# Optimization experiments

Hardware: AMD Instinct MI355X
Metric: run time of the kernel (lower is better)

The kernel has to match this reference:

```python
import jax, jax.numpy as jnp
import numpy as np

NEG = -9e15  # matches -9000000000000000.0 in the torch source


def setup_inputs() -> dict:
    key = jax.random.key(0)
    k1, k2, k3, k4 = jax.random.split(key, 4)
    N, F_in, F_out = 8192, 512, 64
    h = jax.random.normal(k1, (N, F_in), dtype=jnp.float32)
    adj = jax.random.randint(k2, (N, N), 0, 2, dtype=jnp.int32)
    # xavier_uniform with gain=1.414
    def xavier(k, shape, gain=1.414):
        fan_in, fan_out = shape[0], shape[1]
        bound = gain * np.sqrt(6.0 / (fan_in + fan_out))
        return jax.random.uniform(k, shape, dtype=jnp.float32, minval=-bound, maxval=bound)
    W = xavier(k3, (F_in, F_out))
    a = xavier(k4, (2 * F_out, 1))
    return {"h": h, "adj": adj, "W": W, "a": a}


def reference(h, adj, W, a):
    alpha = 0.2
    F_out = W.shape[1]
    Wh = h.astype(jnp.float32) @ W                      # [N, F_out]
    # e[i,j] = leakyrelu( Wh[i] . a[:F_out] + Wh[j] . a[F_out:] )
    Wh1 = Wh @ a[:F_out, :]                             # [N, 1]
    Wh2 = Wh @ a[F_out:, :]                             # [N, 1]
    e = jax.nn.leaky_relu(Wh1 + Wh2.T, negative_slope=alpha)  # [N, N]
    scores = jnp.where(adj > 0, e, NEG)                 # mask non-edges
    attention = jax.nn.softmax(scores, axis=1)          # row softmax
    h_prime = attention @ Wh                            # [N, F_out]
    return h_prime
```

## Files before the change

### kernel.cpp

```cpp
#include <hip/hip_runtime.h>
#include <cstdint>
#include <cstddef>


#define GAT_N    8192
#define GAT_FIN  512
#define GAT_F    64
#define TJ       64
#define JSPLIT   16
#define JCHUNK   (GAT_N / JSPLIT)
#define NTILES   (JCHUNK / TJ)
#define NWORDS   (GAT_N / 64)

typedef __attribute__((ext_vector_type(8))) short short8;
typedef __attribute__((ext_vector_type(4))) float f32x4;

__device__ __forceinline__ float lrelu(float x) { return fmaxf(x, 0.2f * x); }

__device__ __forceinline__ unsigned enc_f32(float f) {
    unsigned b = __float_as_uint(f);
    return b ^ ((b & 0x80000000u) ? 0xFFFFFFFFu : 0x80000000u);
}
__device__ __forceinline__ float dec_f32(unsigned u) {
    return __uint_as_float(u ^ ((u & 0x80000000u) ? 0x80000000u : 0xFFFFFFFFu));
}
__device__ __forceinline__ short f2bf_trunc(float f) {
    return (short)(__float_as_uint(f) >> 16);
}
__device__ __forceinline__ float bfhi(float f) {
    return __uint_as_float(__float_as_uint(f) & 0xFFFF0000u);
}

__device__ __forceinline__ void gload_lds16(const void* g, void* l) {
    __builtin_amdgcn_global_load_lds(
        (const __attribute__((address_space(1))) void*)g,
        (__attribute__((address_space(3))) void*)l, 16, 0, 0);
}

__global__ __launch_bounds__(256) void k_pack(
    const int* __restrict__ adj, unsigned long long* __restrict__ packed)
{
    const int lane = threadIdx.x & 63;
    const int wv   = blockIdx.x * 4 + (threadIdx.x >> 6);
    const size_t wbase = (size_t)wv * 256;
    for (int it = 0; it < 32; ++it) {
        const size_t w0 = wbase + (size_t)it * 8;
        const int* src = adj + w0 * 64 + lane;
        unsigned long long b0, b1, b2, b3, b4, b5, b6, b7;
        b0 = __ballot(src[0 * 64] > 0);
        b1 = __ballot(src[1 * 64] > 0);
        b2 = __ballot(src[2 * 64] > 0);
        b3 = __ballot(src[3 * 64] > 0);
        b4 = __ballot(src[4 * 64] > 0);
        b5 = __ballot(src[5 * 64] > 0);
        b6 = __ballot(src[6 * 64] > 0);
        b7 = __ballot(src[7 * 64] > 0);
        if (lane == 0) {
            ulonglong2* dst = (ulonglong2*)&packed[w0];
            dst[0] = {b0, b1};
            dst[1] = {b2, b3};
            dst[2] = {b4, b5};
            dst[3] = {b6, b7};
        }
    }
}

__global__ __launch_bounds__(256) void k_wh(
    const float* __restrict__ h, const float* __restrict__ W,
    const float* __restrict__ a,
    float* __restrict__ wh1, float* __restrict__ wh2,
    unsigned int* __restrict__ mw2,
    unsigned short* __restrict__ whtHi, unsigned short* __restrict__ whtLo)
{
    __shared__ float sW[2][64 * GAT_F];
    __shared__ unsigned short sTh[GAT_F][16];
    __shared__ unsigned short sTl[GAT_F][16];
    __shared__ unsigned int smax[16];
    const int tid  = threadIdx.x;
    const int lane = tid & 63;
    const int wq   = __builtin_amdgcn_readfirstlane(tid >> 6);
    const size_t r0 = (size_t)blockIdx.x * 16;
    const int rp = tid >> 4;
    const int f4 = (tid & 15) * 4;

    int Bg[4];
#pragma unroll
    for (int c = 0; c < 4; ++c) Bg[c] = wq * 64 + c * 256;

    const char* wsrc = (const char*)W;
    {
        char* dst = (char*)sW[0];
#pragma unroll
        for (int c = 0; c < 4; ++c)
            gload_lds16(wsrc + (size_t)(Bg[c] + lane) * 16, dst + Bg[c] * 16);
    }

    const float* ha = h + (r0 + rp) * GAT_FIN;
    float4 acc = {0.f, 0.f, 0.f, 0.f};

    for (int ck = 0; ck < 8; ++ck) {
        __syncthreads();
        if (ck + 1 < 8) {
            const char* src = wsrc + (size_t)(ck + 1) * 16384;
            char* dst = (char*)sW[(ck + 1) & 1];
#pragma unroll
            for (int c = 0; c < 4; ++c)
                gload_lds16(src + (size_t)(Bg[c] + lane) * 16, dst + Bg[c] * 16);
        }
        const float* wcp = sW[ck & 1];
#pragma unroll 4
        for (int k4 = 0; k4 < 16; ++k4) {
            float4 hv = *(const float4*)&ha[ck * 64 + k4 * 4];
            const float* hvf = (const float*)&hv;
#pragma unroll
            for (int kk = 0; kk < 4; ++kk) {
                float4 wv = *(const float4*)&wcp[(k4 * 4 + kk) * GAT_F + f4];
                acc.x = fmaf(hvf[kk], wv.x, acc.x);
                acc.y = fmaf(hvf[kk], wv.y, acc.y);
                acc.z = fmaf(hvf[kk], wv.z, acc.z);
                acc.w = fmaf(hvf[kk], wv.w, acc.w);
            }
        }
    }

    float4 a1 = *(const float4*)&a[f4];
    float4 a2 = *(const float4*)&a[GAT_F + f4];
    float pa = acc.x*a1.x + acc.y*a1.y + acc.z*a1.z + acc.w*a1.w;
    float pb = acc.x*a2.x + acc.y*a2.y + acc.z*a2.z + acc.w*a2.w;
#pragma unroll
    for (int m = 1; m < 16; m <<= 1) {
        pa += __shfl_xor(pa, m);
        pb += __shfl_xor(pb, m);
    }
    if ((tid & 15) == 0) {
        wh1[r0 + rp] = pa;
        wh2[r0 + rp] = pb;
        smax[rp] = enc_f32(pb);
    }

    const float* af = (const float*)&acc;
#pragma unroll
    for (int e = 0; e < 4; ++e) {
        float v = af[e];
        sTh[f4 + e][rp] = (unsigned short)f2bf_trunc(v);
        sTl[f4 + e][rp] = (unsigned short)f2bf_trunc(v - bfhi(v));
    }
    __syncthreads();

    {
        const int f = tid >> 2, rq = tid & 3;
        uint2 vh = *(const uint2*)&sTh[f][rq * 4];
        uint2 vl = *(const uint2*)&sTl[f][rq * 4];
        *(uint2*)&whtHi[(size_t)f * GAT_N + r0 + rq * 4] = vh;
        *(uint2*)&whtLo[(size_t)f * GAT_N + r0 + rq * 4] = vl;
    }
    if (tid == 0) {
        unsigned m = smax[0];
#pragma unroll
        for (int r = 1; r < 16; ++r) m = max(m, smax[r]);
        atomicMax(mw2, m);
    }
}

__global__ __launch_bounds__(256, 4) void k_attend(
    const unsigned long long* __restrict__ packed,
    const unsigned short* __restrict__ whtHi,
    const unsigned short* __restrict__ whtLo,
    const float* __restrict__ wh1, const float* __restrict__ wh2,
    const unsigned int* __restrict__ mw2,
    float* __restrict__ po, float* __restrict__ pl)
{
    __shared__ char sB[2][16384];

    const int tid  = threadIdx.x;
    const int w    = tid >> 6;
    const int lane = tid & 63;
    const int wq   = __builtin_amdgcn_readfirstlane(w);
    const int fl   = lane & 15;
    const int jg   = lane >> 4;
    const int rw   = blockIdx.x * 64 + w * 16;
    const int j0   = blockIdx.y * JCHUNK;

    const float Mw2 = dec_f32(*mw2);
    const float ai  = wh1[rw + fl];
    const float Mi  = lrelu(ai + Mw2);

    const char* ssrc[4]; int sdstu[4];
#pragma unroll
    for (int c = 0; c < 4; ++c) {
        const int Bgc = wq * 64 + (c & 1) * 256;
        const int G   = Bgc + lane;
        const int f = G >> 3, g = G & 7;
        const unsigned short* base = (c < 2) ? whtHi : whtLo;
        ssrc[c]  = (const char*)(base + (size_t)f * GAT_N + j0 + ((g ^ (f & 7)) * 8));
        sdstu[c] = ((c < 2) ? 0 : 8192) + Bgc * 16;
    }

    const int off0 = fl * 128 + (((0 * 4 + jg) ^ (fl & 7)) * 16);
    const int off1 = fl * 128 + (((1 * 4 + jg) ^ (fl & 7)) * 16);

    const unsigned long long* mp = packed + (size_t)(rw + fl) * NWORDS + (j0 >> 6);
    const float* wp = wh2 + j0 + jg * 8;

    {
#pragma unroll
        for (int c = 0; c < 4; ++c)
            gload_lds16(ssrc[c], (char*)sB[0] + sdstu[c]);
    }
    unsigned long long amc = mp[0];
    float4 wc[4];
#pragma unroll
    for (int q = 0; q < 4; ++q)
        wc[q] = *(const float4*)(wp + (q >> 1) * 32 + (q & 1) * 4);

    f32x4 acc[4] = {};
    float psum = 0.f;

    for (int t = 0; t < NTILES; ++t) {
        const int cur = t & 1;
        __syncthreads();

        if (t + 1 < NTILES) {
#pragma unroll
            for (int c = 0; c < 4; ++c)
                gload_lds16(ssrc[c] + (size_t)(t + 1) * 128,
                            (char*)sB[cur ^ 1] + sdstu[c]);
        }
        const int tn = (t + 1 < NTILES) ? t + 1 : t;
        unsigned long long amn = mp[tn];
        float4 wn[4];
#pragma unroll
        for (int q = 0; q < 4; ++q)
            wn[q] = *(const float4*)(wp + tn * TJ + (q >> 1) * 32 + (q & 1) * 4);

        const char* sbc = sB[cur];
#pragma unroll
        for (int s = 0; s < 2; ++s) {
            const unsigned m8 = (unsigned)(amc >> (s * 32 + jg * 8)) & 0xFFu;
            float pv[8];
#pragma unroll
            for (int hh = 0; hh < 2; ++hh) {
                const float* bvf = (const float*)&wc[s * 2 + hh];
#pragma unroll
                for (int e = 0; e < 4; ++e) {
                    float sc = lrelu(ai + bvf[e]);
                    float pe = __expf(sc - Mi);
                    pv[hh * 4 + e] = ((m8 >> (hh * 4 + e)) & 1u) ? pe : 0.f;
                }
            }
            short8 ph, plo;
#pragma unroll
            for (int e = 0; e < 8; ++e) {
                psum  += pv[e];
                ph[e]  = f2bf_trunc(pv[e]);
                plo[e] = f2bf_trunc(pv[e] - bfhi(pv[e]));
            }
            const int offs = s ? off1 : off0;
#pragma unroll
            for (int nb = 0; nb < 4; ++nb) {
                short8 bh = *(const short8*)(sbc + offs + nb * 2048);
                short8 bl = *(const short8*)(sbc + 8192 + offs + nb * 2048);
                acc[nb] = __builtin_amdgcn_mfma_f32_16x16x32_bf16(ph,  bh, acc[nb], 0, 0, 0);
                acc[nb] = __builtin_amdgcn_mfma_f32_16x16x32_bf16(plo, bh, acc[nb], 0, 0, 0);
                acc[nb] = __builtin_amdgcn_mfma_f32_16x16x32_bf16(ph,  bl, acc[nb], 0, 0, 0);
            }
        }
        amc = amn;
#pragma unroll
        for (int q = 0; q < 4; ++q) wc[q] = wn[q];
    }

    psum += __shfl_xor(psum, 16);
    psum += __shfl_xor(psum, 32);
    if (lane < 16)
        pl[(size_t)blockIdx.y * GAT_N + rw + lane] = psum;

    const size_t ob = ((size_t)blockIdx.y * GAT_N + rw + jg * 4) * GAT_F + fl;
#pragma unroll
    for (int nb = 0; nb < 4; ++nb) {
#pragma unroll
        for (int r = 0; r < 4; ++r)
            po[ob + (size_t)r * GAT_F + nb * 16] = acc[nb][r];
    }
}

__global__ __launch_bounds__(256) void k_merge(
    const float* __restrict__ po, const float* __restrict__ pl,
    float* __restrict__ out)
{
    const int idx = blockIdx.x * 256 + threadIdx.x;
    const int i = idx >> 6;
    float s = 0.f, ls = 0.f;
#pragma unroll
    for (int y = 0; y < JSPLIT; ++y) {
        s  += po[(size_t)y * GAT_N * GAT_F + idx];
        ls += pl[(size_t)y * GAT_N + i];
    }
    out[idx] = s / ls;
}

extern "C" void kernel_launch(void* const* d_in, const int* in_sizes, int n_in,
                              void* d_out, int out_size, void* d_ws, size_t ws_size,
                              hipStream_t stream) {
    (void)in_sizes; (void)n_in; (void)out_size; (void)ws_size;
    const float* h   = (const float*)d_in[0];
    const int*   adj = (const int*)d_in[1];
    const float* W   = (const float*)d_in[2];
    const float* a   = (const float*)d_in[3];
    float* out = (float*)d_out;

    char* wsb = (char*)d_ws;
    float*              wh1    = (float*)(wsb);
    float*              wh2    = (float*)(wsb + 32768);
    unsigned int*       mw2    = (unsigned int*)(wsb + 65536);
    unsigned long long* packed = (unsigned long long*)(wsb + 131072);
    unsigned short*     whtHi  = (unsigned short*)(wsb + 8519680);
    unsigned short*     whtLo  = (unsigned short*)(wsb + 9568256);
    float*              po     = (float*)(wsb + 10616832);
    float*              pl     = (float*)(wsb + 44171264);

    hipMemsetAsync(mw2, 0, 4, stream);
    k_pack  <<<1024, 256, 0, stream>>>(adj, packed);
    k_wh    <<<GAT_N / 16, 256, 0, stream>>>(h, W, a, wh1, wh2, mw2, whtHi, whtLo);
    k_attend<<<dim3(GAT_N / 64, JSPLIT), 256, 0, stream>>>(packed, whtHi, whtLo,
                                                           wh1, wh2, mw2, po, pl);
    k_merge <<<GAT_N * GAT_F / 256, 256, 0, stream>>>(po, pl, out);
}
```

Before: 451.6 us.

## Pre-pack Wh into MFMA fragment layout and load B operands directly from global

```diff
diff --git a/kernel.cpp b/kernel.cpp
--- a/kernel.cpp
+++ b/kernel.cpp
@@ -35,6 +35,10 @@
     __builtin_amdgcn_global_load_lds(
         (const __attribute__((address_space(1))) void*)g,
         (__attribute__((address_space(3))) void*)l, 16, 0, 0);
+}
+
+__device__ __forceinline__ short8 as_short8(const int4& v) {
+    union { int4 i; short8 s; } u; u.i = v; return u.s;
 }
 
 __global__ __launch_bounds__(256) void k_pack(
@@ -70,7 +74,7 @@
     const float* __restrict__ a,
     float* __restrict__ wh1, float* __restrict__ wh2,
     unsigned int* __restrict__ mw2,
-    unsigned short* __restrict__ whtHi, unsigned short* __restrict__ whtLo)
+    char* __restrict__ pbHi, char* __restrict__ pbLo)
 {
     __shared__ float sW[2][64 * GAT_F];
     __shared__ unsigned short sTh[GAT_F][16];
@@ -148,11 +152,21 @@
     __syncthreads();
 
     {
-        const int f = tid >> 2, rq = tid & 3;
-        uint2 vh = *(const uint2*)&sTh[f][rq * 4];
-        uint2 vl = *(const uint2*)&sTl[f][rq * 4];
-        *(uint2*)&whtHi[(size_t)f * GAT_N + r0 + rq * 4] = vh;
-        *(uint2*)&whtLo[(size_t)f * GAT_N + r0 + rq * 4] = vl;
+        const int tt  = blockIdx.x >> 2;
+        const int q   = blockIdx.x & 3;
+        const int s   = q >> 1;
+        const int hf  = tid >> 7;
+        const int rem = tid & 127;
+        const int nb  = rem >> 5;
+        const int jgo = (rem >> 4) & 1;
+        const int fl  = rem & 15;
+        const int jga = (q & 1) * 2 + jgo;
+        const unsigned short* st = hf ? &sTl[nb * 16 + fl][jgo * 8]
+                                      : &sTh[nb * 16 + fl][jgo * 8];
+        uint4 v = *(const uint4*)st;
+        char* base = hf ? pbLo : pbHi;
+        *(uint4*)(base + (size_t)tt * 8192 + s * 4096 + nb * 1024
+                       + (jga * 16 + fl) * 16) = v;
     }
     if (tid == 0) {
         unsigned m = smax[0];
@@ -162,20 +176,16 @@
     }
 }
 
-__global__ __launch_bounds__(256, 4) void k_attend(
+__global__ __launch_bounds__(256, 3) void k_attend(
     const unsigned long long* __restrict__ packed,
-    const unsigned short* __restrict__ whtHi,
-    const unsigned short* __restrict__ whtLo,
+    const char* __restrict__ pbHi, const char* __restrict__ pbLo,
     const float* __restrict__ wh1, const float* __restrict__ wh2,
     const unsigned int* __restrict__ mw2,
     float* __restrict__ po, float* __restrict__ pl)
 {
-    __shared__ char sB[2][16384];
-
     const int tid  = threadIdx.x;
     const int w    = tid >> 6;
     const int lane = tid & 63;
-    const int wq   = __builtin_amdgcn_readfirstlane(w);
     const int fl   = lane & 15;
     const int jg   = lane >> 4;
     const int rw   = blockIdx.x * 64 + w * 16;
@@ -185,68 +195,48 @@
     const float ai  = wh1[rw + fl];
     const float Mi  = lrelu(ai + Mw2);
 
-    const char* ssrc[4]; int sdstu[4];
-#pragma unroll
-    for (int c = 0; c < 4; ++c) {
-        const int Bgc = wq * 64 + (c & 1) * 256;
-        const int G   = Bgc + lane;
-        const int f = G >> 3, g = G & 7;
-        const unsigned short* base = (c < 2) ? whtHi : whtLo;
-        ssrc[c]  = (const char*)(base + (size_t)f * GAT_N + j0 + ((g ^ (f & 7)) * 8));
-        sdstu[c] = ((c < 2) ? 0 : 8192) + Bgc * 16;
-    }
-
-    const int off0 = fl * 128 + (((0 * 4 + jg) ^ (fl & 7)) * 16);
-    const int off1 = fl * 128 + (((1 * 4 + jg) ^ (fl & 7)) * 16);
+    const char* bh0 = pbHi + (size_t)(j0 >> 6) * 8192 + lane * 16;
+    const char* bl0 = pbLo + (size_t)(j0 >> 6) * 8192 + lane * 16;
 
     const unsigned long long* mp = packed + (size_t)(rw + fl) * NWORDS + (j0 >> 6);
     const float* wp = wh2 + j0 + jg * 8;
 
-    {
-#pragma unroll
-        for (int c = 0; c < 4; ++c)
-            gload_lds16(ssrc[c], (char*)sB[0] + sdstu[c]);
+    int4 B0h[4], B0l[4], B1h[4], B1l[4];
+#pragma unroll
+    for (int nb = 0; nb < 4; ++nb) {
+        B0h[nb] = *(const int4*)(bh0 + nb * 1024);
+        B0l[nb] = *(const int4*)(bl0 + nb * 1024);
     }
     unsigned long long amc = mp[0];
-    float4 wc[4];
-#pragma unroll
-    for (int q = 0; q < 4; ++q)
-        wc[q] = *(const float4*)(wp + (q >> 1) * 32 + (q & 1) * 4);
 
     f32x4 acc[4] = {};
     float psum = 0.f;
 
     for (int t = 0; t < NTILES; ++t) {
-        const int cur = t & 1;
-        __syncthreads();
-
-        if (t + 1 < NTILES) {
-#pragma unroll
-            for (int c = 0; c < 4; ++c)
-                gload_lds16(ssrc[c] + (size_t)(t + 1) * 128,
-                            (char*)sB[cur ^ 1] + sdstu[c]);
-        }
         const int tn = (t + 1 < NTILES) ? t + 1 : t;
         unsigned long long amn = mp[tn];
-        float4 wn[4];
-#pragma unroll
-        for (int q = 0; q < 4; ++q)
-            wn[q] = *(const float4*)(wp + tn * TJ + (q >> 1) * 32 + (q & 1) * 4);
-
-        const char* sbc = sB[cur];
-#pragma unroll
-        for (int s = 0; s < 2; ++s) {
-            const unsigned m8 = (unsigned)(amc >> (s * 32 + jg * 8)) & 0xFFu;
+
+        {
+            const char* bh = bh0 + t * 8192 + 4096;
+            const char* bl = bl0 + t * 8192 + 4096;
+#pragma unroll
+            for (int nb = 0; nb < 4; ++nb) {
+                B1h[nb] = *(const int4*)(bh + nb * 1024);
+                B1l[nb] = *(const int4*)(bl + nb * 1024);
+            }
+        }
+
+        {
+            const float4 wA = *(const float4*)(wp + t * TJ);
+            const float4 wB = *(const float4*)(wp + t * TJ + 4);
+            const unsigned m8 = (unsigned)(amc >> (jg * 8)) & 0xFFu;
             float pv[8];
-#pragma unroll
-            for (int hh = 0; hh < 2; ++hh) {
-                const float* bvf = (const float*)&wc[s * 2 + hh];
-#pragma unroll
-                for (int e = 0; e < 4; ++e) {
-                    float sc = lrelu(ai + bvf[e]);
-                    float pe = __expf(sc - Mi);
-                    pv[hh * 4 + e] = ((m8 >> (hh * 4 + e)) & 1u) ? pe : 0.f;
-                }
+            const float* wAf = (const float*)&wA;
+            const float* wBf = (const float*)&wB;
+#pragma unroll
+            for (int e = 0; e < 4; ++e) {
+                pv[e]     = ((m8 >> e) & 1u)       ? __expf(lrelu(ai + wAf[e]) - Mi) : 0.f;
+                pv[4 + e] = ((m8 >> (4 + e)) & 1u) ? __expf(lrelu(ai + wBf[e]) - Mi) : 0.f;
             }
             short8 ph, plo;
 #pragma unroll
@@ -255,19 +245,56 @@
                 ph[e]  = f2bf_trunc(pv[e]);
                 plo[e] = f2bf_trunc(pv[e] - bfhi(pv[e]));
             }
-            const int offs = s ? off1 : off0;
 #pragma unroll
             for (int nb = 0; nb < 4; ++nb) {
-                short8 bh = *(const short8*)(sbc + offs + nb * 2048);
-                short8 bl = *(const short8*)(sbc + 8192 + offs + nb * 2048);
+                short8 bh = as_short8(B0h[nb]);
+                short8 bl = as_short8(B0l[nb]);
                 acc[nb] = __builtin_amdgcn_mfma_f32_16x16x32_bf16(ph,  bh, acc[nb], 0, 0, 0);
                 acc[nb] = __builtin_amdgcn_mfma_f32_16x16x32_bf16(plo, bh, acc[nb], 0, 0, 0);
                 acc[nb] = __builtin_amdgcn_mfma_f32_16x16x32_bf16(ph,  bl, acc[nb], 0, 0, 0);
             }
         }
+
+        {
+            const char* bh = bh0 + tn * 8192;
+            const char* bl = bl0 + tn * 8192;
+#pragma unroll
+            for (int nb = 0; nb < 4; ++nb) {
+                B0h[nb] = *(const int4*)(bh + nb * 1024);
+                B0l[nb] = *(const int4*)(bl + nb * 1024);
+            }
+        }
+
+        {
+            const float4 wA = *(const float4*)(wp + t * TJ + 32);
+            const float4 wB = *(const float4*)(wp + t * TJ + 36);
+            const unsigned m8 = (unsigned)(amc >> (32 + jg * 8)) & 0xFFu;
+            float pv[8];
+            const float* wAf = (const float*)&wA;
+            const float* wBf = (const float*)&wB;
+#pragma unroll
+            for (int e = 0; e < 4; ++e) {
+                pv[e]     = ((m8 >> e) & 1u)       ? __expf(lrelu(ai + wAf[e]) - Mi) : 0.f;
+                pv[4 + e] = ((m8 >> (4 + e)) & 1u) ? __expf(lrelu(ai + wBf[e]) - Mi) : 0.f;
+            }
+            short8 ph, plo;
+#pragma unroll
+            for (int e = 0; e < 8; ++e) {
+                psum  += pv[e];
+                ph[e]  = f2bf_trunc(pv[e]);
+                plo[e] = f2bf_trunc(pv[e] - bfhi(pv[e]));
+            }
+#pragma unroll
+            for (int nb = 0; nb < 4; ++nb) {
+                short8 bh = as_short8(B1h[nb]);
+                short8 bl = as_short8(B1l[nb]);
+                acc[nb] = __builtin_amdgcn_mfma_f32_16x16x32_bf16(ph,  bh, acc[nb], 0, 0, 0);
+                acc[nb] = __builtin_amdgcn_mfma_f32_16x16x32_bf16(plo, bh, acc[nb], 0, 0, 0);
+                acc[nb] = __builtin_amdgcn_mfma_f32_16x16x32_bf16(ph,  bl, acc[nb], 0, 0, 0);
+            }
+        }
+
         amc = amn;
-#pragma unroll
-        for (int q = 0; q < 4; ++q) wc[q] = wn[q];
     }
 
     psum += __shfl_xor(psum, 16);
@@ -314,15 +341,15 @@
     float*              wh2    = (float*)(wsb + 32768);
     unsigned int*       mw2    = (unsigned int*)(wsb + 65536);
     unsigned long long* packed = (unsigned long long*)(wsb + 131072);
-    unsigned short*     whtHi  = (unsigned short*)(wsb + 8519680);
-    unsigned short*     whtLo  = (unsigned short*)(wsb + 9568256);
+    char*               pbHi   = (wsb + 8519680);
+    char*               pbLo   = (wsb + 9568256);
     float*              po     = (float*)(wsb + 10616832);
     float*              pl     = (float*)(wsb + 44171264);
 
     hipMemsetAsync(mw2, 0, 4, stream);
     k_pack  <<<1024, 256, 0, stream>>>(adj, packed);
-    k_wh    <<<GAT_N / 16, 256, 0, stream>>>(h, W, a, wh1, wh2, mw2, whtHi, whtLo);
-    k_attend<<<dim3(GAT_N / 64, JSPLIT), 256, 0, stream>>>(packed, whtHi, whtLo,
+    k_wh    <<<GAT_N / 16, 256, 0, stream>>>(h, W, a, wh1, wh2, mw2, pbHi, pbLo);
+    k_attend<<<dim3(GAT_N / 64, JSPLIT), 256, 0, stream>>>(packed, pbHi, pbLo,
                                                            wh1, wh2, mw2, po, pl);
     k_merge <<<GAT_N * GAT_F / 256, 256, 0, stream>>>(po, pl, out);
 }
```

Measured after the change: 525.1 us. 1.16x slower.
